# Optimization experiments

Measured on AMD Instinct MI355X. Metric: run time of the kernel, lower is better.

## Reference

```python
import jax, jax.numpy as jnp
import numpy as np

N = 100000
E = 640000
D_IN = 128
D_OUT = 128


def setup_inputs() -> dict:
    key = jax.random.key(0)
    k1, k2, k3, k4, k5 = jax.random.split(key, 5)
    x = jax.random.normal(k1, (N, D_IN), dtype=jnp.float32)
    edge_index = jax.random.randint(k2, (2, E), 0, N, dtype=jnp.int64)
    edge_weight = jax.random.uniform(k3, (E,), dtype=jnp.float32)
    W_rel = jax.random.normal(k4, (D_OUT, D_IN), dtype=jnp.float32) / np.sqrt(D_IN)
    W_root = jax.random.normal(k5, (D_OUT, D_IN), dtype=jnp.float32) / np.sqrt(D_IN)
    b = jnp.zeros((D_OUT,), dtype=jnp.float32)
    return {"x": x, "edge_index": edge_index, "edge_weight": edge_weight,
            "W_rel": W_rel, "W_root": W_root, "b": b}


def reference(x, edge_index, edge_weight, W_rel, W_root, b):
    # PyG GraphConv: out_i = W_rel @ (sum_{j -> i} w_ij * x_j) + W_root @ x_i + b
    src = edge_index[0]  # message source (x_j)
    dst = edge_index[1]  # aggregation target
    msg = x[src] * edge_weight[:, None]          # [E, D_IN] gather + scale
    agg = jax.ops.segment_sum(msg, dst, num_segments=x.shape[0])  # [N, D_IN]
    out = agg @ W_rel.T + x @ W_root.T + b       # [N, D_OUT]
    return out
```

## Files before the change

kernel.cpp:

```cpp
#include <hip/hip_runtime.h>
#include <hip/hip_fp16.h>

#define NN 100000
#define EE 640000
#define D 128
#define NBINS NN
#define SCAN_NBLK 98

#define BKT 1563
#define EBLK 256
#define EPB 2500

#define WS_LCNT     0
#define WS_TOT      400128
#define WS_BOFFS    401728
#define WS_OFFS     403328
#define WS_SW       503360
#define WS_SW2      1783360
#define WS_WF       3063360
#define WS_XH       3079744
#define WS_AGGD     9479744
#define WS_INTS_TOP 15879744

#define WS_CNTM     0
#define WS_OFFSM    100000
#define WS_BSUMM    200000
#define WS_SWM      200192
#define WS_WCONV    1480192
#define WS_INTS_MID 1512960

#define PREP_XB 3125
#define PREP_WB 128
#define PREP_AB EBLK

typedef __attribute__((ext_vector_type(8))) short    short8v;
typedef __attribute__((ext_vector_type(8))) _Float16 half8v;
typedef __attribute__((ext_vector_type(4))) float    floatx4;
struct __align__(8) half4t { __half2 a, b; };

__device__ inline void split_bf16(float f, short& h, short& l) {
    unsigned u  = __float_as_uint(f);
    unsigned hb = u & 0xFFFF0000u;
    h = (short)(u >> 16);
    float fl = f - __uint_as_float(hb);
    l = (short)(__float_as_uint(fl) >> 16);
}

__global__ __launch_bounds__(256) void scatter_kernel(
    const float* __restrict__ x, const int* __restrict__ ei,
    const float* __restrict__ ew, float* agg)
{
    int gid = blockIdx.x * 256 + threadIdx.x;
    int e = gid >> 7, f = gid & 127;
    if (e >= EE) return;
    float v = x[ei[e] * D + f] * ew[e];
    unsafeAtomicAdd(&agg[ei[EE + e] * D + f], v);
}

__global__ __launch_bounds__(256) void prepA_kernel(
    const float* __restrict__ x, const float* __restrict__ Wrel,
    const float* __restrict__ Wroot, const int* __restrict__ ei,
    short* __restrict__ xh, short* __restrict__ Wf, int* __restrict__ lcnt)
{
    __shared__ int h[BKT];
    const int b = blockIdx.x;
    if (b < PREP_XB) {
        const int base = b * 4096 + threadIdx.x * 4;
        float4 v[4];
        #pragma unroll
        for (int u = 0; u < 4; u++)
            v[u] = *(const float4*)&x[base + u * 1024];
        #pragma unroll
        for (int u = 0; u < 4; u++) {
            short4 hh;
            hh.x = (short)__half_as_ushort(__float2half(v[u].x));
            hh.y = (short)__half_as_ushort(__float2half(v[u].y));
            hh.z = (short)__half_as_ushort(__float2half(v[u].z));
            hh.w = (short)__half_as_ushort(__float2half(v[u].w));
            *(short4*)&xh[base + u * 1024] = hh;
        }
    } else if (b < PREP_XB + PREP_WB) {
        int i = (b - PREP_XB) * 256 + threadIdx.x;
        int c = i >> 8, k = i & 255;
        float f = (k < 128) ? Wrel[c * 128 + k] : Wroot[c * 128 + (k - 128)];
        Wf[i] = (short)__half_as_ushort(__float2half(f));
    } else {
        const int eb = b - PREP_XB - PREP_WB;
        for (int i = threadIdx.x; i < BKT; i += 256) h[i] = 0;
        __syncthreads();
        const int e0 = eb * EPB, e1 = e0 + EPB;
        for (int e = e0 + threadIdx.x; e < e1; e += 256)
            atomicAdd(&h[ei[EE + e] >> 6], 1);
        __syncthreads();
        for (int i = threadIdx.x; i < BKT; i += 256)
            lcnt[eb * BKT + i] = h[i];
    }
}

__global__ __launch_bounds__(256) void colscan_kernel(
    int* __restrict__ lcnt, int* __restrict__ tot)
{
    int t = blockIdx.x * 256 + threadIdx.x;
    if (t >= BKT) return;
    int run = 0;
    for (int b = 0; b < EBLK; b++) {
        int v = lcnt[b * BKT + t];
        lcnt[b * BKT + t] = run;
        run += v;
    }
    tot[t] = run;
}

__global__ __launch_bounds__(256) void scanT_kernel(
    const int* __restrict__ tot, int* __restrict__ boffs)
{
    __shared__ int s[256];
    __shared__ int carry;
    if (threadIdx.x == 0) carry = 0;
    __syncthreads();
    for (int c = 0; c < 7; c++) {
        int idx = c * 256 + threadIdx.x;
        int v = (idx < BKT) ? tot[idx] : 0;
        s[threadIdx.x] = v;
        __syncthreads();
        for (int off = 1; off < 256; off <<= 1) {
            int t = (threadIdx.x >= off) ? s[threadIdx.x - off] : 0;
            __syncthreads();
            s[threadIdx.x] += t;
            __syncthreads();
        }
        if (idx < BKT) boffs[idx] = carry + s[threadIdx.x] - v;
        __syncthreads();
        if (threadIdx.x == 0) carry += s[255];
        __syncthreads();
    }
    if (threadIdx.x == 0) boffs[BKT] = EE;
}

__global__ __launch_bounds__(256) void passB_kernel(
    const int* __restrict__ ei, const float* __restrict__ ew,
    const int* __restrict__ lcnt, const int* __restrict__ boffs,
    int2* __restrict__ sw)
{
    __shared__ int base2[BKT];
    __shared__ int cur[BKT];
    const int eb = blockIdx.x;
    for (int i = threadIdx.x; i < BKT; i += 256) {
        base2[i] = boffs[i] + lcnt[eb * BKT + i];
        cur[i] = 0;
    }
    __syncthreads();
    const int e0 = eb * EPB, e1 = e0 + EPB;
    for (int e = e0 + threadIdx.x; e < e1; e += 256) {
        int src = ei[e];
        int dst = ei[EE + e];
        int bkt = dst >> 6;
        int r = atomicAdd(&cur[bkt], 1);
        sw[base2[bkt] + r] = make_int2(src | ((dst & 63) << 17),
                                       __float_as_int(ew[e]));
    }
}

__global__ __launch_bounds__(256) void passC_kernel(
    const int2* __restrict__ sw, const int* __restrict__ boffs,
    int2* __restrict__ sw2, int* __restrict__ offs)
{
    __shared__ int cnt[64], nb[64], cur[64];
    __shared__ int segbeg, segend;
    const int bkt = blockIdx.x;
    if (threadIdx.x == 0) { segbeg = boffs[bkt]; segend = boffs[bkt + 1]; }
    if (threadIdx.x < 64) { cnt[threadIdx.x] = 0; cur[threadIdx.x] = 0; }
    __syncthreads();
    for (int j = segbeg + threadIdx.x; j < segend; j += 256)
        atomicAdd(&cnt[(sw[j].x >> 17) & 63], 1);
    __syncthreads();
    if (threadIdx.x < 64) nb[threadIdx.x] = cnt[threadIdx.x];
    __syncthreads();
    for (int off = 1; off < 64; off <<= 1) {
        int t = 0;
        if (threadIdx.x < 64 && threadIdx.x >= off) t = nb[threadIdx.x - off];
        __syncthreads();
        if (threadIdx.x < 64) nb[threadIdx.x] += t;
        __syncthreads();
    }
    if (threadIdx.x < 64) {
        int b = segbeg + nb[threadIdx.x] - cnt[threadIdx.x];
        nb[threadIdx.x] = b;
        int node = bkt * 64 + threadIdx.x;
        if (node < NN) offs[node] = b;
    }
    __syncthreads();
    for (int j = segbeg + threadIdx.x; j < segend; j += 256) {
        int2 v = sw[j];
        int n = (v.x >> 17) & 63;
        int r = atomicAdd(&cur[n], 1);
        sw2[nb[n] + r] = make_int2(v.x & 0x1FFFF, v.y);
    }
    if (bkt == 0 && threadIdx.x == 0) offs[NN] = EE;
}

__global__ __launch_bounds__(256) void aggregate_h_kernel(
    const short* __restrict__ xh, const int* __restrict__ offs,
    const int2* __restrict__ sw2, short* __restrict__ aggd)
{
    const int node = blockIdx.x * 8 + (threadIdx.x >> 5);
    const int fl   = threadIdx.x & 31;
    if (node >= NN) return;
    const int beg = offs[node];
    const int end = offs[node + 1];
    const half4t* xp = (const half4t*)xh;

    float4 a0 = make_float4(0.f, 0.f, 0.f, 0.f);
    float4 a1 = make_float4(0.f, 0.f, 0.f, 0.f);
    int j = beg;
    for (; j + 3 < end; j += 4) {
        int2 s0 = sw2[j], s1 = sw2[j + 1], s2 = sw2[j + 2], s3 = sw2[j + 3];
        half4t v0 = xp[(size_t)s0.x * 32 + fl];
        half4t v1 = xp[(size_t)s1.x * 32 + fl];
        half4t v2 = xp[(size_t)s2.x * 32 + fl];
        half4t v3 = xp[(size_t)s3.x * 32 + fl];
        float w0 = __int_as_float(s0.y), w1 = __int_as_float(s1.y);
        float w2 = __int_as_float(s2.y), w3 = __int_as_float(s3.y);
        float2 l0 = __half22float2(v0.a), h0 = __half22float2(v0.b);
        float2 l1 = __half22float2(v1.a), h1 = __half22float2(v1.b);
        float2 l2 = __half22float2(v2.a), h2 = __half22float2(v2.b);
        float2 l3 = __half22float2(v3.a), h3 = __half22float2(v3.b);
        a0.x += w0 * l0.x; a0.y += w0 * l0.y; a0.z += w0 * h0.x; a0.w += w0 * h0.y;
        a1.x += w1 * l1.x; a1.y += w1 * l1.y; a1.z += w1 * h1.x; a1.w += w1 * h1.y;
        a0.x += w2 * l2.x; a0.y += w2 * l2.y; a0.z += w2 * h2.x; a0.w += w2 * h2.y;
        a1.x += w3 * l3.x; a1.y += w3 * l3.y; a1.z += w3 * h3.x; a1.w += w3 * h3.y;
    }
    for (; j + 1 < end; j += 2) {
        int2 s0 = sw2[j], s1 = sw2[j + 1];
        half4t v0 = xp[(size_t)s0.x * 32 + fl];
        half4t v1 = xp[(size_t)s1.x * 32 + fl];
        float w0 = __int_as_float(s0.y), w1 = __int_as_float(s1.y);
        float2 l0 = __half22float2(v0.a), h0 = __half22float2(v0.b);
        float2 l1 = __half22float2(v1.a), h1 = __half22float2(v1.b);
        a0.x += w0 * l0.x; a0.y += w0 * l0.y; a0.z += w0 * h0.x; a0.w += w0 * h0.y;
        a1.x += w1 * l1.x; a1.y += w1 * l1.y; a1.z += w1 * h1.x; a1.w += w1 * h1.y;
    }
    if (j < end) {
        int2 s0 = sw2[j];
        half4t v0 = xp[(size_t)s0.x * 32 + fl];
        float w0 = __int_as_float(s0.y);
        float2 l0 = __half22float2(v0.a), h0 = __half22float2(v0.b);
        a0.x += w0 * l0.x; a0.y += w0 * l0.y; a0.z += w0 * h0.x; a0.w += w0 * h0.y;
    }
    float4 r = make_float4(a0.x + a1.x, a0.y + a1.y, a0.z + a1.z, a0.w + a1.w);
    half4t o;
    o.a = __floats2half2_rn(r.x, r.y);
    o.b = __floats2half2_rn(r.z, r.w);
    ((half4t*)aggd)[(size_t)node * 32 + fl] = o;
}

__global__ __launch_bounds__(256) void mfma_f16_kernel(
    const short* __restrict__ xh, const short* __restrict__ aggd,
    const short* __restrict__ Wf, const float* __restrict__ bias,
    float* __restrict__ out)
{
    __shared__ short lds[2 * 128 * 64];
    short* At = lds;
    short* Wt = lds + 8192;

    const int tid  = threadIdx.x;
    const int lane = tid & 63;
    const int wave = tid >> 6;
    const int row0 = blockIdx.x * 128;
    const int frow = lane & 15;

    floatx4 acc[2][8];
    #pragma unroll
    for (int nf = 0; nf < 8; nf++) {
        float b = bias[nf * 16 + frow];
        #pragma unroll
        for (int mf = 0; mf < 2; mf++) acc[mf][nf] = (floatx4){b, b, b, b};
    }

    for (int kc = 0; kc < 4; kc++) {
        const short* A = (kc < 2) ? aggd : xh;
        const int kcol = (kc & 1) * 64;
        __syncthreads();
        #pragma unroll
        for (int i = 0; i < 4; i++) {
            int e = (i * 256 + tid) * 8;
            int r = e >> 6, k = e & 63;
            int rg = row0 + r;
            short8v v = (short8v)0;
            if (rg < NN) v = *(const short8v*)&A[(size_t)rg * 128 + kcol + k];
            int sidx = r * 64 + (((k >> 3) ^ (r & 7)) << 3);
            *(short8v*)&At[sidx] = v;
        }
        #pragma unroll
        for (int i = 0; i < 4; i++) {
            int e = (i * 256 + tid) * 8;
            int c = e >> 6, k = e & 63;
            int sidx = c * 64 + (((k >> 3) ^ (c & 7)) << 3);
            *(short8v*)&Wt[sidx] = *(const short8v*)&Wf[c * 256 + kc * 64 + k];
        }
        __syncthreads();

        const int arow = wave * 32;
        #pragma unroll
        for (int kf = 0; kf < 2; kf++) {
            const int kblk = kf * 4 + (lane >> 4);
            half8v a[2];
            #pragma unroll
            for (int mf = 0; mf < 2; mf++) {
                int r = arow + mf * 16 + frow;
                int idx = r * 64 + ((kblk ^ (r & 7)) << 3);
                a[mf] = *(const half8v*)&At[idx];
            }
            #pragma unroll
            for (int nf = 0; nf < 8; nf++) {
                int cc = nf * 16 + frow;
                int idx = cc * 64 + ((kblk ^ (cc & 7)) << 3);
                half8v b = *(const half8v*)&Wt[idx];
                #pragma unroll
                for (int mf = 0; mf < 2; mf++)
                    acc[mf][nf] = __builtin_amdgcn_mfma_f32_16x16x32_f16(a[mf], b, acc[mf][nf], 0, 0, 0);
            }
        }
    }

    const int orow = row0 + wave * 32;
    #pragma unroll
    for (int mf = 0; mf < 2; mf++) {
        #pragma unroll
        for (int j = 0; j < 4; j++) {
            int r = orow + mf * 16 + (lane >> 4) * 4 + j;
            if (r < NN) {
                #pragma unroll
                for (int nf = 0; nf < 8; nf++)
                    out[(size_t)r * D + nf * 16 + (lane & 15)] = acc[mf][nf][j];
            }
        }
    }
}

__global__ __launch_bounds__(256) void zero_cnt_kernel(int* __restrict__ cnt)
{
    int i = blockIdx.x * 256 + threadIdx.x;
    if (i < NBINS) cnt[i] = 0;
}

__global__ __launch_bounds__(256) void hist_kernel(
    const int* __restrict__ ei, int* __restrict__ cnt)
{
    int e = blockIdx.x * 256 + threadIdx.x;
    if (e < EE) atomicAdd(&cnt[ei[EE + e]], 1);
}

__global__ __launch_bounds__(256) void wconv_kernel(
    const float* __restrict__ Wrel, const float* __restrict__ Wroot,
    short* __restrict__ Wb)
{
    int i = blockIdx.x * 256 + threadIdx.x;
    int c = i >> 8, k = i & 255;
    float f = (k < 128) ? Wrel[c * 128 + k] : Wroot[c * 128 + (k - 128)];
    short h, l;
    split_bf16(f, h, l);
    Wb[i] = h;
    Wb[32768 + i] = l;
}

__global__ __launch_bounds__(256) void scanA_kernel(
    const int* __restrict__ cnt, int* __restrict__ offs, int* __restrict__ bsum)
{
    __shared__ int tsum[256];
    const int tid = threadIdx.x;
    const int base = blockIdx.x * 1024 + tid * 4;
    int v[4], s = 0;
    #pragma unroll
    for (int i = 0; i < 4; i++) {
        int idx = base + i;
        v[i] = (idx < NBINS) ? cnt[idx] : 0;
        s += v[i];
    }
    tsum[tid] = s;
    __syncthreads();
    for (int off = 1; off < 256; off <<= 1) {
        int t = (tid >= off) ? tsum[tid - off] : 0;
        __syncthreads();
        tsum[tid] += t;
        __syncthreads();
    }
    int run = tsum[tid] - s;
    #pragma unroll
    for (int i = 0; i < 4; i++) {
        int idx = base + i;
        if (idx < NBINS) offs[idx] = run;
        run += v[i];
    }
    if (tid == 255) bsum[blockIdx.x] = tsum[255];
}

__global__ __launch_bounds__(256) void scanC_kernel(
    int* __restrict__ offs, const int* __restrict__ bsum)
{
    __shared__ int s[128];
    const int tid = threadIdx.x;
    if (tid < 128) s[tid] = (tid < SCAN_NBLK) ? bsum[tid] : 0;
    __syncthreads();
    for (int off = 1; off < 128; off <<= 1) {
        int t = 0;
        if (tid < 128 && tid >= off) t = s[tid - off];
        __syncthreads();
        if (tid < 128) s[tid] += t;
        __syncthreads();
    }
    const int add = (blockIdx.x == 0) ? 0 : s[blockIdx.x - 1];
    const int base = blockIdx.x * 1024 + tid * 4;
    #pragma unroll
    for (int i = 0; i < 4; i++) {
        int idx = base + i;
        if (idx < NBINS) offs[idx] += add;
    }
}

__global__ __launch_bounds__(256) void buildM_kernel(
    const int* __restrict__ ei, const float* __restrict__ ew,
    int* __restrict__ offs, int2* __restrict__ sw)
{
    int e = blockIdx.x * 256 + threadIdx.x;
    if (e >= EE) return;
    int dst = ei[EE + e];
    int p = atomicAdd(&offs[dst], 1);
    sw[p] = make_int2(ei[e], __float_as_int(ew[e]));
}

__global__ __launch_bounds__(256) void aggregate_kernel(
    const float* __restrict__ x, const int* __restrict__ offs,
    const int2* __restrict__ sw, float* __restrict__ out)
{
    const int node = blockIdx.x * 8 + (threadIdx.x >> 5);
    const int fl   = threadIdx.x & 31;
    if (node >= NN) return;
    const int beg = (node == 0) ? 0 : offs[node - 1];
    const int end = offs[node];
    const float4* x4 = (const float4*)x;

    float4 a0 = make_float4(0.f, 0.f, 0.f, 0.f);
    float4 a1 = make_float4(0.f, 0.f, 0.f, 0.f);
    int j = beg;
    for (; j + 1 < end; j += 2) {
        int2 s0 = sw[j];
        int2 s1 = sw[j + 1];
        float4 v0 = x4[(size_t)s0.x * 32 + fl];
        float4 v1 = x4[(size_t)s1.x * 32 + fl];
        float w0 = __int_as_float(s0.y), w1 = __int_as_float(s1.y);
        a0.x += w0 * v0.x; a0.y += w0 * v0.y; a0.z += w0 * v0.z; a0.w += w0 * v0.w;
        a1.x += w1 * v1.x; a1.y += w1 * v1.y; a1.z += w1 * v1.z; a1.w += w1 * v1.w;
    }
    if (j < end) {
        int2 s0 = sw[j];
        float4 v0 = x4[(size_t)s0.x * 32 + fl];
        float w0 = __int_as_float(s0.y);
        a0.x += w0 * v0.x; a0.y += w0 * v0.y; a0.z += w0 * v0.z; a0.w += w0 * v0.w;
    }
    float4 r = make_float4(a0.x + a1.x, a0.y + a1.y, a0.z + a1.z, a0.w + a1.w);
    ((float4*)out)[(size_t)node * 32 + fl] = r;
}

__global__ __launch_bounds__(256) void mfma_gemm_kernel(
    const float* __restrict__ x, const short* __restrict__ Wb,
    const float* __restrict__ bias, float* __restrict__ out)
{
    __shared__ short lds[4 * 128 * 64];
    short* Ah = lds;
    short* Al = lds + 8192;
    short* Wh = lds + 16384;
    short* Wl = lds + 24576;

    const int tid  = threadIdx.x;
    const int lane = tid & 63;
    const int wave = tid >> 6;
    const int row0 = blockIdx.x * 128;
    const int frow = lane & 15;
    const int fk   = (lane >> 4) * 8;

    floatx4 acc[2][8];
    #pragma unroll
    for (int nf = 0; nf < 8; nf++) {
        float b = bias[nf * 16 + frow];
        #pragma unroll
        for (int mf = 0; mf < 2; mf++) acc[mf][nf] = (floatx4){b, b, b, b};
    }

    for (int kc = 0; kc < 4; kc++) {
        const float* A = (kc < 2) ? out : x;
        const int kcol = (kc & 1) * 64;
        __syncthreads();
        #pragma unroll
        for (int i = 0; i < 8; i++) {
            int e = (i * 256 + tid) * 4;
            int r = e >> 6, k = e & 63;
            int rg = row0 + r;
            float4 v = (rg < NN) ? *(const float4*)&A[(size_t)rg * D + kcol + k]
                                 : make_float4(0.f, 0.f, 0.f, 0.f);
            short4 h, l;
            split_bf16(v.x, h.x, l.x);
            split_bf16(v.y, h.y, l.y);
            split_bf16(v.z, h.z, l.z);
            split_bf16(v.w, h.w, l.w);
            int sidx = r * 64 + (((k >> 3) ^ (r & 7)) << 3) + (k & 7);
            *(short4*)&Ah[sidx] = h;
            *(short4*)&Al[sidx] = l;
        }
        #pragma unroll
        for (int i = 0; i < 4; i++) {
            int e = (i * 256 + tid) * 8;
            int c = e >> 6, k = e & 63;
            int sidx = c * 64 + (((k >> 3) ^ (c & 7)) << 3);
            int g = c * 256 + kc * 64 + k;
            *(short8v*)&Wh[sidx] = *(const short8v*)&Wb[g];
            *(short8v*)&Wl[sidx] = *(const short8v*)&Wb[32768 + g];
        }
        __syncthreads();

        const int arow = wave * 32;
        #pragma unroll
        for (int kf = 0; kf < 2; kf++) {
            const int kblk = (kf * 32 + fk) >> 3;
            short8v ah[2], al[2];
            #pragma unroll
            for (int mf = 0; mf < 2; mf++) {
                int r = arow + mf * 16 + frow;
                int idx = r * 64 + ((kblk ^ (r & 7)) << 3);
                ah[mf] = *(const short8v*)&Ah[idx];
                al[mf] = *(const short8v*)&Al[idx];
            }
            #pragma unroll
            for (int nf = 0; nf < 8; nf++) {
                int cc = nf * 16 + frow;
                int idx = cc * 64 + ((kblk ^ (cc & 7)) << 3);
                short8v bh = *(const short8v*)&Wh[idx];
                short8v bl = *(const short8v*)&Wl[idx];
                #pragma unroll
                for (int mf = 0; mf < 2; mf++) {
                    acc[mf][nf] = __builtin_amdgcn_mfma_f32_16x16x32_bf16(ah[mf], bh, acc[mf][nf], 0, 0, 0);
                    acc[mf][nf] = __builtin_amdgcn_mfma_f32_16x16x32_bf16(al[mf], bh, acc[mf][nf], 0, 0, 0);
                    acc[mf][nf] = __builtin_amdgcn_mfma_f32_16x16x32_bf16(ah[mf], bl, acc[mf][nf], 0, 0, 0);
                }
            }
        }
    }

    const int orow = row0 + wave * 32;
    #pragma unroll
    for (int mf = 0; mf < 2; mf++) {
        #pragma unroll
        for (int j = 0; j < 4; j++) {
            int r = orow + mf * 16 + (lane >> 4) * 4 + j;
            if (r < NN) {
                #pragma unroll
                for (int nf = 0; nf < 8; nf++)
                    out[(size_t)r * D + nf * 16 + (lane & 15)] = acc[mf][nf][j];
            }
        }
    }
}

__global__ __launch_bounds__(512) void gemm_kernel(
    const float* __restrict__ x, const float* __restrict__ Wrel,
    const float* __restrict__ Wroot, const float* __restrict__ bias,
    float* out)
{
    __shared__ float AtT[128][65];
    const int tid  = threadIdx.x;
    const int lane = tid & 63;
    const int wid  = __builtin_amdgcn_readfirstlane(tid >> 6);
    const int row0 = blockIdx.x * 64;
    float acc[16];
    {
        const float* bb = bias + wid * 16;
        #pragma unroll
        for (int c = 0; c < 16; c++) acc[c] = bb[c];
    }
    for (int phase = 0; phase < 2; phase++) {
        const float* A = phase ? x : out;
        const float* W = (phase ? Wroot : Wrel) + wid * 16 * D;
        __syncthreads();
        #pragma unroll
        for (int i = 0; i < 16; i++) {
            int e = i * 512 + tid;
            int r = e >> 7, k = e & 127;
            int rg = row0 + r;
            AtT[k][r] = (rg < NN) ? A[rg * D + k] : 0.0f;
        }
        __syncthreads();
        for (int k4 = 0; k4 < 32; k4++) {
            float a0 = AtT[k4 * 4 + 0][lane];
            float a1 = AtT[k4 * 4 + 1][lane];
            float a2 = AtT[k4 * 4 + 2][lane];
            float a3 = AtT[k4 * 4 + 3][lane];
            #pragma unroll
            for (int c = 0; c < 16; c++) {
                const float* wp = W + c * D + k4 * 4;
                acc[c] += a0 * wp[0] + a1 * wp[1] + a2 * wp[2] + a3 * wp[3];
            }
        }
    }
    __syncthreads();
    #pragma unroll
    for (int c = 0; c < 16; c++)
        AtT[wid * 16 + c][lane] = acc[c];
    __syncthreads();
    #pragma unroll
    for (int i = 0; i < 16; i++) {
        int e = i * 512 + tid;
        int r = e >> 7, col = e & 127;
        int rg = row0 + r;
        if (rg < NN) out[rg * D + col] = AtT[col][r];
    }
}

extern "C" void kernel_launch(void* const* d_in, const int* in_sizes, int n_in,
                              void* d_out, int out_size, void* d_ws, size_t ws_size,
                              hipStream_t stream) {
    const float* x     = (const float*)d_in[0];
    const int*   ei    = (const int*)  d_in[1];
    const float* ew    = (const float*)d_in[2];
    const float* Wrel  = (const float*)d_in[3];
    const float* Wroot = (const float*)d_in[4];
    const float* bias  = (const float*)d_in[5];
    float*       out   = (float*)d_out;

    const int eb = (EE + 255) / 256;

    if (ws_size >= (size_t)WS_INTS_TOP * sizeof(int)) {
        int* w = (int*)d_ws;
        int*   lcnt  = w + WS_LCNT;
        int*   tot   = w + WS_TOT;
        int*   boffs = w + WS_BOFFS;
        int*   offs  = w + WS_OFFS;
        int2*  sw    = (int2*)(w + WS_SW);
        int2*  sw2   = (int2*)(w + WS_SW2);
        short* Wf    = (short*)(w + WS_WF);
        short* xh    = (short*)(w + WS_XH);
        short* aggd  = (short*)(w + WS_AGGD);

        prepA_kernel<<<PREP_XB + PREP_WB + PREP_AB, 256, 0, stream>>>(
            x, Wrel, Wroot, ei, xh, Wf, lcnt);
        colscan_kernel<<<(BKT + 255) / 256, 256, 0, stream>>>(lcnt, tot);
        scanT_kernel<<<1, 256, 0, stream>>>(tot, boffs);
        passB_kernel<<<EBLK, 256, 0, stream>>>(ei, ew, lcnt, boffs, sw);
        passC_kernel<<<BKT, 256, 0, stream>>>(sw, boffs, sw2, offs);
        aggregate_h_kernel<<<NN / 8, 256, 0, stream>>>(xh, offs, sw2, aggd);
        mfma_f16_kernel<<<(NN + 127) / 128, 256, 0, stream>>>(xh, aggd, Wf, bias, out);
    } else if (ws_size >= (size_t)WS_INTS_MID * sizeof(int)) {
        int* w = (int*)d_ws;
        int*   cnt  = w + WS_CNTM;
        int*   offs = w + WS_OFFSM;
        int*   bsum = w + WS_BSUMM;
        int2*  sw   = (int2*)(w + WS_SWM);
        short* Wb   = (short*)(w + WS_WCONV);

        zero_cnt_kernel<<<(NBINS + 255) / 256, 256, 0, stream>>>(cnt);
        wconv_kernel<<<128, 256, 0, stream>>>(Wrel, Wroot, Wb);
        hist_kernel <<<eb, 256, 0, stream>>>(ei, cnt);
        scanA_kernel<<<SCAN_NBLK, 256, 0, stream>>>(cnt, offs, bsum);
        scanC_kernel<<<SCAN_NBLK, 256, 0, stream>>>(offs, bsum);
        buildM_kernel<<<eb, 256, 0, stream>>>(ei, ew, offs, sw);
        aggregate_kernel<<<NN / 8, 256, 0, stream>>>(x, offs, sw, out);
        mfma_gemm_kernel<<<(NN + 127) / 128, 256, 0, stream>>>(x, Wb, bias, out);
    } else {
        hipMemsetAsync(out, 0, (size_t)NN * D * sizeof(float), stream);
        scatter_kernel<<<(EE * 128) / 256, 256, 0, stream>>>(x, ei, ew, out);
        gemm_kernel<<<(NN + 63) / 64, 512, 0, stream>>>(x, Wrel, Wroot, bias, out);
    }
}
```

Baseline: 116.7 us.

## Fuse neighbor aggregation into MFMA GEMM kernel via LDS staging

Merges the separate aggregation and GEMM kernels into one: each 128-row block first gathers and sums its neighbors' fp16 features into a swizzled LDS tile, then runs the MFMA GEMM reading the aggregate half of the A operand straight from LDS. This drops the global write and re-read of the fp16 aggregate buffer and one kernel launch. In exchange only 782 blocks do the gather (16 serial rows per half-wave), so memory-latency-bound gather parallelism falls sharply, and LDS use rises to 64KB per block, which limits occupancy.

```diff
diff --git a/kernel.cpp b/kernel.cpp
--- a/kernel.cpp
+++ b/kernel.cpp
@@ -19,8 +19,7 @@
 #define WS_SW2      1783360
 #define WS_WF       3063360
 #define WS_XH       3079744
-#define WS_AGGD     9479744
-#define WS_INTS_TOP 15879744
+#define WS_INTS_TOP 9479744
 
 #define WS_CNTM     0
 #define WS_OFFSM    100000
@@ -199,69 +198,14 @@
     if (bkt == 0 && threadIdx.x == 0) offs[NN] = EE;
 }
 
-__global__ __launch_bounds__(256) void aggregate_h_kernel(
+__global__ __launch_bounds__(256) void fused_agg_gemm_kernel(
     const short* __restrict__ xh, const int* __restrict__ offs,
-    const int2* __restrict__ sw2, short* __restrict__ aggd)
-{
-    const int node = blockIdx.x * 8 + (threadIdx.x >> 5);
-    const int fl   = threadIdx.x & 31;
-    if (node >= NN) return;
-    const int beg = offs[node];
-    const int end = offs[node + 1];
-    const half4t* xp = (const half4t*)xh;
-
-    float4 a0 = make_float4(0.f, 0.f, 0.f, 0.f);
-    float4 a1 = make_float4(0.f, 0.f, 0.f, 0.f);
-    int j = beg;
-    for (; j + 3 < end; j += 4) {
-        int2 s0 = sw2[j], s1 = sw2[j + 1], s2 = sw2[j + 2], s3 = sw2[j + 3];
-        half4t v0 = xp[(size_t)s0.x * 32 + fl];
-        half4t v1 = xp[(size_t)s1.x * 32 + fl];
-        half4t v2 = xp[(size_t)s2.x * 32 + fl];
-        half4t v3 = xp[(size_t)s3.x * 32 + fl];
-        float w0 = __int_as_float(s0.y), w1 = __int_as_float(s1.y);
-        float w2 = __int_as_float(s2.y), w3 = __int_as_float(s3.y);
-        float2 l0 = __half22float2(v0.a), h0 = __half22float2(v0.b);
-        float2 l1 = __half22float2(v1.a), h1 = __half22float2(v1.b);
-        float2 l2 = __half22float2(v2.a), h2 = __half22float2(v2.b);
-        float2 l3 = __half22float2(v3.a), h3 = __half22float2(v3.b);
-        a0.x += w0 * l0.x; a0.y += w0 * l0.y; a0.z += w0 * h0.x; a0.w += w0 * h0.y;
-        a1.x += w1 * l1.x; a1.y += w1 * l1.y; a1.z += w1 * h1.x; a1.w += w1 * h1.y;
-        a0.x += w2 * l2.x; a0.y += w2 * l2.y; a0.z += w2 * h2.x; a0.w += w2 * h2.y;
-        a1.x += w3 * l3.x; a1.y += w3 * l3.y; a1.z += w3 * h3.x; a1.w += w3 * h3.y;
-    }
-    for (; j + 1 < end; j += 2) {
-        int2 s0 = sw2[j], s1 = sw2[j + 1];
-        half4t v0 = xp[(size_t)s0.x * 32 + fl];
-        half4t v1 = xp[(size_t)s1.x * 32 + fl];
-        float w0 = __int_as_float(s0.y), w1 = __int_as_float(s1.y);
-        float2 l0 = __half22float2(v0.a), h0 = __half22float2(v0.b);
-        float2 l1 = __half22float2(v1.a), h1 = __half22float2(v1.b);
-        a0.x += w0 * l0.x; a0.y += w0 * l0.y; a0.z += w0 * h0.x; a0.w += w0 * h0.y;
-        a1.x += w1 * l1.x; a1.y += w1 * l1.y; a1.z += w1 * h1.x; a1.w += w1 * h1.y;
-    }
-    if (j < end) {
-        int2 s0 = sw2[j];
-        half4t v0 = xp[(size_t)s0.x * 32 + fl];
-        float w0 = __int_as_float(s0.y);
-        float2 l0 = __half22float2(v0.a), h0 = __half22float2(v0.b);
-        a0.x += w0 * l0.x; a0.y += w0 * l0.y; a0.z += w0 * h0.x; a0.w += w0 * h0.y;
-    }
-    float4 r = make_float4(a0.x + a1.x, a0.y + a1.y, a0.z + a1.z, a0.w + a1.w);
-    half4t o;
-    o.a = __floats2half2_rn(r.x, r.y);
-    o.b = __floats2half2_rn(r.z, r.w);
-    ((half4t*)aggd)[(size_t)node * 32 + fl] = o;
-}
-
-__global__ __launch_bounds__(256) void mfma_f16_kernel(
-    const short* __restrict__ xh, const short* __restrict__ aggd,
-    const short* __restrict__ Wf, const float* __restrict__ bias,
-    float* __restrict__ out)
-{
-    __shared__ short lds[2 * 128 * 64];
-    short* At = lds;
-    short* Wt = lds + 8192;
+    const int2* __restrict__ sw2, const short* __restrict__ Wf,
+    const float* __restrict__ bias, float* __restrict__ out)
+{
+    __shared__ short aggT[16384];
+    __shared__ short At[8192];
+    __shared__ short Wt[8192];
 
     const int tid  = threadIdx.x;
     const int lane = tid & 63;
@@ -269,6 +213,63 @@
     const int row0 = blockIdx.x * 128;
     const int frow = lane & 15;
 
+    {
+        const int hw = tid >> 5;
+        const int fl = tid & 31;
+        const int ac = fl >> 4;
+        const int klocal = (fl * 4) & 63;
+        const half4t* xp = (const half4t*)xh;
+        for (int t = 0; t < 16; t++) {
+            const int r = hw * 16 + t;
+            const int node = row0 + r;
+            float4 a0 = make_float4(0.f, 0.f, 0.f, 0.f);
+            float4 a1 = make_float4(0.f, 0.f, 0.f, 0.f);
+            if (node < NN) {
+                const int beg = offs[node], end = offs[node + 1];
+                int j = beg;
+                for (; j + 3 < end; j += 4) {
+                    int2 s0 = sw2[j], s1 = sw2[j + 1], s2 = sw2[j + 2], s3 = sw2[j + 3];
+                    half4t v0 = xp[(size_t)s0.x * 32 + fl];
+                    half4t v1 = xp[(size_t)s1.x * 32 + fl];
+                    half4t v2 = xp[(size_t)s2.x * 32 + fl];
+                    half4t v3 = xp[(size_t)s3.x * 32 + fl];
+                    float w0 = __int_as_float(s0.y), w1 = __int_as_float(s1.y);
+                    float w2 = __int_as_float(s2.y), w3 = __int_as_float(s3.y);
+                    float2 l0 = __half22float2(v0.a), h0 = __half22float2(v0.b);
+                    float2 l1 = __half22float2(v1.a), h1 = __half22float2(v1.b);
+                    float2 l2 = __half22float2(v2.a), h2 = __half22float2(v2.b);
+                    float2 l3 = __half22float2(v3.a), h3 = __half22float2(v3.b);
+                    a0.x += w0 * l0.x; a0.y += w0 * l0.y; a0.z += w0 * h0.x; a0.w += w0 * h0.y;
+                    a1.x += w1 * l1.x; a1.y += w1 * l1.y; a1.z += w1 * h1.x; a1.w += w1 * h1.y;
+                    a0.x += w2 * l2.x; a0.y += w2 * l2.y; a0.z += w2 * h2.x; a0.w += w2 * h2.y;
+                    a1.x += w3 * l3.x; a1.y += w3 * l3.y; a1.z += w3 * h3.x; a1.w += w3 * h3.y;
+                }
+                for (; j + 1 < end; j += 2) {
+                    int2 s0 = sw2[j], s1 = sw2[j + 1];
+                    half4t v0 = xp[(size_t)s0.x * 32 + fl];
+                    half4t v1 = xp[(size_t)s1.x * 32 + fl];
+                    float w0 = __int_as_float(s0.y), w1 = __int_as_float(s1.y);
+                    float2 l0 = __half22float2(v0.a), h0 = __half22float2(v0.b);
+                    float2 l1 = __half22float2(v1.a), h1 = __half22float2(v1.b);
+                    a0.x += w0 * l0.x; a0.y += w0 * l0.y; a0.z += w0 * h0.x; a0.w += w0 * h0.y;
+                    a1.x += w1 * l1.x; a1.y += w1 * l1.y; a1.z += w1 * h1.x; a1.w += w1 * h1.y;
+                }
+                if (j < end) {
+                    int2 s0 = sw2[j];
+                    half4t v0 = xp[(size_t)s0.x * 32 + fl];
+                    float w0 = __int_as_float(s0.y);
+                    float2 l0 = __half22float2(v0.a), h0 = __half22float2(v0.b);
+                    a0.x += w0 * l0.x; a0.y += w0 * l0.y; a0.z += w0 * h0.x; a0.w += w0 * h0.y;
+                }
+            }
+            half4t o;
+            o.a = __floats2half2_rn(a0.x + a1.x, a0.y + a1.y);
+            o.b = __floats2half2_rn(a0.z + a1.z, a0.w + a1.w);
+            int sidx = ac * 8192 + r * 64 + (((klocal >> 3) ^ (r & 7)) << 3) + (klocal & 7);
+            *(half4t*)&aggT[sidx] = o;
+        }
+    }
+
     floatx4 acc[2][8];
     #pragma unroll
     for (int nf = 0; nf < 8; nf++) {
@@ -278,18 +279,19 @@
     }
 
     for (int kc = 0; kc < 4; kc++) {
-        const short* A = (kc < 2) ? aggd : xh;
-        const int kcol = (kc & 1) * 64;
-        __syncthreads();
-        #pragma unroll
-        for (int i = 0; i < 4; i++) {
-            int e = (i * 256 + tid) * 8;
-            int r = e >> 6, k = e & 63;
-            int rg = row0 + r;
-            short8v v = (short8v)0;
-            if (rg < NN) v = *(const short8v*)&A[(size_t)rg * 128 + kcol + k];
-            int sidx = r * 64 + (((k >> 3) ^ (r & 7)) << 3);
-            *(short8v*)&At[sidx] = v;
+        __syncthreads();
+        if (kc >= 2) {
+            #pragma unroll
+            for (int i = 0; i < 4; i++) {
+                int e = (i * 256 + tid) * 8;
+                int r = e >> 6, k = e & 63;
+                int rg = row0 + r;
+                short8v v = (short8v)0;
+                if (rg < NN)
+                    v = *(const short8v*)&xh[(size_t)rg * 128 + (kc - 2) * 64 + k];
+                int sidx = r * 64 + (((k >> 3) ^ (r & 7)) << 3);
+                *(short8v*)&At[sidx] = v;
+            }
         }
         #pragma unroll
         for (int i = 0; i < 4; i++) {
@@ -300,6 +302,7 @@
         }
         __syncthreads();
 
+        const short* Asrc = (kc < 2) ? &aggT[kc * 8192] : At;
         const int arow = wave * 32;
         #pragma unroll
         for (int kf = 0; kf < 2; kf++) {
@@ -309,7 +312,7 @@
             for (int mf = 0; mf < 2; mf++) {
                 int r = arow + mf * 16 + frow;
                 int idx = r * 64 + ((kblk ^ (r & 7)) << 3);
-                a[mf] = *(const half8v*)&At[idx];
+                a[mf] = *(const half8v*)&Asrc[idx];
             }
             #pragma unroll
             for (int nf = 0; nf < 8; nf++) {
@@ -638,7 +641,6 @@
         int2*  sw2   = (int2*)(w + WS_SW2);
         short* Wf    = (short*)(w + WS_WF);
         short* xh    = (short*)(w + WS_XH);
-        short* aggd  = (short*)(w + WS_AGGD);
 
         prepA_kernel<<<PREP_XB + PREP_WB + PREP_AB, 256, 0, stream>>>(
             x, Wrel, Wroot, ei, xh, Wf, lcnt);
@@ -646,8 +648,8 @@
         scanT_kernel<<<1, 256, 0, stream>>>(tot, boffs);
         passB_kernel<<<EBLK, 256, 0, stream>>>(ei, ew, lcnt, boffs, sw);
         passC_kernel<<<BKT, 256, 0, stream>>>(sw, boffs, sw2, offs);
-        aggregate_h_kernel<<<NN / 8, 256, 0, stream>>>(xh, offs, sw2, aggd);
-        mfma_f16_kernel<<<(NN + 127) / 128, 256, 0, stream>>>(xh, aggd, Wf, bias, out);
+        fused_agg_gemm_kernel<<<(NN + 127) / 128, 256, 0, stream>>>(
+            xh, offs, sw2, Wf, bias, out);
     } else if (ws_size >= (size_t)WS_INTS_MID * sizeof(int)) {
         int* w = (int*)d_ws;
         int*   cnt  = w + WS_CNTM;
```

Result: slower. 162.1 us (+38.9%).
